# Optimization experiments

Hardware: AMD Instinct MI355X
Metric: run time of the kernel (lower is better)

## Reference

```python
import jax, jax.numpy as jnp
import numpy as np

N_NODES = 50000
N_EDGES = 800000
IN_DIM = 128
HID = 64
OUT = 64
HEADS = 4
NEG_SLOPE = 0.2  # DGL GATConv default leaky_relu negative slope


def gat_conv(x, src, dst, W, attn_l, attn_r, bias, n_heads, d_out, n_nodes):
    """DGL-style GATConv: x [N, F_in] -> [N, H, D]."""
    feat = (x @ W).reshape(n_nodes, n_heads, d_out)            # [N,H,D]
    el = jnp.sum(feat * attn_l, axis=-1)                        # [N,H]
    er = jnp.sum(feat * attn_r, axis=-1)                        # [N,H]
    e = jax.nn.leaky_relu(el[src] + er[dst], NEG_SLOPE)         # [E,H]
    # edge softmax over incoming edges of each dst node
    emax = jax.ops.segment_max(e, dst, num_segments=n_nodes)    # [N,H]
    emax = jnp.where(jnp.isfinite(emax), emax, 0.0)
    emax = jax.lax.stop_gradient(emax)
    a = jnp.exp(e - emax[dst])                                  # [E,H]
    denom = jax.ops.segment_sum(a, dst, num_segments=n_nodes)   # [N,H]
    alpha = a / jnp.maximum(denom[dst], 1e-9)                   # [E,H]
    msg = feat[src] * alpha[:, :, None]                         # [E,H,D]
    out = jax.ops.segment_sum(msg, dst, num_segments=n_nodes)   # [N,H,D]
    return out + bias.reshape(1, n_heads, d_out)


def setup_inputs() -> dict:
    key = jax.random.key(0)
    ks = jax.random.split(key, 12)
    features = jax.random.normal(ks[0], (N_NODES, IN_DIM), jnp.float32)
    src = jax.random.randint(ks[1], (N_EDGES,), 0, N_NODES)
    dst = jax.random.randint(ks[2], (N_EDGES,), 0, N_NODES)
    s1 = 1.0 / np.sqrt(IN_DIM)
    s2 = 1.0 / np.sqrt(HID * HEADS)
    return {
        "features": features,
        "src": src,
        "dst": dst,
        "W1": jax.random.normal(ks[3], (IN_DIM, HEADS * HID), jnp.float32) * s1,
        "al1": jax.random.normal(ks[4], (HEADS, HID), jnp.float32) * s1,
        "ar1": jax.random.normal(ks[5], (HEADS, HID), jnp.float32) * s1,
        "b1": jnp.zeros((HEADS * HID,), jnp.float32),
        "W2": jax.random.normal(ks[6], (HEADS * HID, HEADS * OUT), jnp.float32) * s2,
        "al2": jax.random.normal(ks[7], (HEADS, OUT), jnp.float32) * s2,
        "ar2": jax.random.normal(ks[8], (HEADS, OUT), jnp.float32) * s2,
        "b2": jnp.zeros((HEADS * OUT,), jnp.float32),
    }


def reference(features, src, dst, W1, al1, ar1, b1, W2, al2, ar2, b2):
    h = gat_conv(features, src, dst, W1, al1, ar1, b1, HEADS, HID, N_NODES)
    h = jax.nn.elu(h)                        # layer1 activation=F.elu
    h = h.reshape(N_NODES, HEADS * HID)      # .flatten(1)
    # dropout(0.2) is identity in eval mode
    h = gat_conv(h, src, dst, W2, al2, ar2, b2, HEADS, OUT, N_NODES)
    return h.mean(axis=1)                    # mean over heads -> [N, OUT]
```

## Files before the change

kernel.cpp:

```cpp
#include <hip/hip_runtime.h>
#include <hip/hip_bf16.h>
#include <math.h>

#define N_NODES 50000
#define N_EDGES 800000
#define IN_DIM 128
#define NEG_SLOPE 0.2f

typedef __attribute__((ext_vector_type(8))) short s16x8;
typedef __attribute__((ext_vector_type(4))) float f32x4;

__device__ inline unsigned short f2bf(float v) {
    unsigned u = __float_as_uint(v);
    unsigned r = (u + 0x7fffu + ((u >> 16) & 1u)) >> 16;
    return (unsigned short)r;
}
__device__ inline float bf2f(unsigned short b) {
    return __uint_as_float(((unsigned)b) << 16);
}
__device__ inline float lrelu(float v) {
    return v >= 0.f ? v : NEG_SLOPE * v;
}


__global__ void zero_int(int* __restrict__ p, int n) {
    int i = blockIdx.x * blockDim.x + threadIdx.x;
    if (i < n) p[i] = 0;
}

__global__ void hist_kernel(const int* __restrict__ dst, int* __restrict__ cnt) {
    int e = blockIdx.x * blockDim.x + threadIdx.x;
    if (e < N_EDGES) atomicAdd(&cnt[dst[e]], 1);
}

__global__ __launch_bounds__(1024) void scan_kernel(const int* __restrict__ cnt,
                                                    int* __restrict__ off, int n) {
    __shared__ int wsum[16];
    __shared__ int carry_s;
    int tid = threadIdx.x, wid = tid >> 6, lane = tid & 63;
    if (tid == 0) carry_s = 0;
    __syncthreads();
    for (int base = 0; base < n; base += 1024) {
        int i = base + tid;
        int v = (i < n) ? cnt[i] : 0;
        int x = v;
#pragma unroll
        for (int s = 1; s < 64; s <<= 1) {
            int t = __shfl_up(x, s, 64);
            if (lane >= s) x += t;
        }
        if (lane == 63) wsum[wid] = x;
        __syncthreads();
        if (wid == 0 && lane < 16) {
            int w = wsum[lane];
#pragma unroll
            for (int s = 1; s < 16; s <<= 1) {
                int t = __shfl_up(w, s, 64);
                if (lane >= s) w += t;
            }
            wsum[lane] = w;
        }
        __syncthreads();
        int woff = (wid > 0) ? wsum[wid - 1] : 0;
        int incl = carry_s + woff + x;
        if (i < n) off[i] = incl - v;
        __syncthreads();
        if (tid == 1023) carry_s = incl;
        __syncthreads();
    }
    if (threadIdx.x == 0) off[n] = carry_s;
}

__global__ void copy_int(const int* __restrict__ a, int* __restrict__ b, int n) {
    int i = blockIdx.x * blockDim.x + threadIdx.x;
    if (i < n) b[i] = a[i];
}

__global__ void scatter_kernel(const int* __restrict__ src, const int* __restrict__ dst,
                               int* __restrict__ cur, int* __restrict__ csr_src) {
    int e = blockIdx.x * blockDim.x + threadIdx.x;
    if (e < N_EDGES) {
        int d = dst[e];
        int pos = atomicAdd(&cur[d], 1);
        csr_src[pos] = src[e];
    }
}


__global__ void split_feat(const float* __restrict__ in, unsigned short* __restrict__ hi,
                           unsigned short* __restrict__ lo, int n4) {
    int i = blockIdx.x * blockDim.x + threadIdx.x;
    if (i < n4) {
        float4 v = *reinterpret_cast<const float4*>(&in[i * 4]);
        ushort4 h, l;
        h.x = f2bf(v.x); l.x = f2bf(v.x - bf2f(h.x));
        h.y = f2bf(v.y); l.y = f2bf(v.y - bf2f(h.y));
        h.z = f2bf(v.z); l.z = f2bf(v.z - bf2f(h.z));
        h.w = f2bf(v.w); l.w = f2bf(v.w - bf2f(h.w));
        *reinterpret_cast<ushort4*>(&hi[i * 4]) = h;
        *reinterpret_cast<ushort4*>(&lo[i * 4]) = l;
    }
}

template <int K>
__global__ void split_wt(const float* __restrict__ W, unsigned short* __restrict__ Bth,
                         unsigned short* __restrict__ Btl) {
    int k = blockIdx.x;
    int c = threadIdx.x;
    int h = c >> 6, w = c & 63;
    int row = h * 64 + (w & 3) * 16 + (w >> 2);
    float v = W[(size_t)k * 256 + c];
    unsigned short hh = f2bf(v);
    Bth[(size_t)row * K + k] = hh;
    Btl[(size_t)row * K + k] = f2bf(v - bf2f(hh));
}

template <int K>
__global__ void wlr_kernel(const float* __restrict__ W, const float* __restrict__ al,
                           const float* __restrict__ ar,
                           unsigned short* __restrict__ EhC, unsigned short* __restrict__ ElC) {
    int k = blockIdx.x * blockDim.x + threadIdx.x;
    if (k >= K) return;
#pragma unroll
    for (int h = 0; h < 4; h++) {
        float sl = 0.f, sr = 0.f;
        for (int c = 0; c < 64; c++) {
            float w = W[(size_t)k * 256 + h * 64 + c];
            sl += w * al[h * 64 + c];
            sr += w * ar[h * 64 + c];
        }
        unsigned short hh = f2bf(sl);
        EhC[(size_t)(h * 2 + 0) * K + k] = hh;
        ElC[(size_t)(h * 2 + 0) * K + k] = f2bf(sl - bf2f(hh));
        hh = f2bf(sr);
        EhC[(size_t)(h * 2 + 1) * K + k] = hh;
        ElC[(size_t)(h * 2 + 1) * K + k] = f2bf(sr - bf2f(hh));
    }
}


#define GLDS(gsrc, loff)                                                        \
    __builtin_amdgcn_global_load_lds(                                           \
        (const __attribute__((address_space(1))) unsigned int*)(gsrc),          \
        (__attribute__((address_space(3))) unsigned int*)(lds + (loff)),        \
        16, 0, 0)

template <int K>
__global__ __launch_bounds__(512) void mfma_gemm(const unsigned short* __restrict__ Ahi,
                                                 const unsigned short* __restrict__ Alo,
                                                 const unsigned short* __restrict__ Bth,
                                                 const unsigned short* __restrict__ Btl,
                                                 const unsigned short* __restrict__ EhC,
                                                 const unsigned short* __restrict__ ElC,
                                                 unsigned short* __restrict__ Chi,
                                                 float* __restrict__ el,
                                                 float* __restrict__ er,
                                                 int M) {
    __shared__ __align__(16) char lds[98304];
    int tid = threadIdx.x;
    int w = tid >> 6;
    int h = w & 3;
    int r2 = w >> 2;
    int lane = tid & 63;
    int rr = lane & 15;
    int g = lane >> 4;
    int row0 = blockIdx.x * 128;

    int arow = row0 + (tid & 127);
    if (arow >= M) arow = M - 1;
    int akc = (tid >> 7) & 3;
    const unsigned short* asrc_h = Ahi + (size_t)arow * K + akc * 8;
    const unsigned short* asrc_l = Alo + (size_t)arow * K + akc * 8;
    int btrow = tid & 255;
    int bkc = (tid >> 8) * 2;
    const unsigned short* bsrc_h = Bth + (size_t)btrow * K + bkc * 8;
    const unsigned short* bsrc_l = Btl + (size_t)btrow * K + bkc * 8;
    int bdst0 = 16384 + bkc * 4096 + btrow * 16;
    int bdst1 = 16384 + (bkc + 1) * 4096 + btrow * 16;

    f32x4 acc[4][4] = {};
    f32x4 acce[4] = {};

    GLDS(asrc_h, tid * 16);
    GLDS(asrc_l, 8192 + tid * 16);
    GLDS(bsrc_h, bdst0);
    GLDS(bsrc_h + 8, bdst1);
    GLDS(bsrc_l, 16384 + bdst0);
    GLDS(bsrc_l + 8, 16384 + bdst1);

    int cur = 0;
    for (int kb = 0; kb < K; kb += 32) {
        __syncthreads();
        if (kb + 32 < K) {
            int nb = (cur ^ 1) * 49152;
            GLDS(asrc_h + kb + 32, nb + tid * 16);
            GLDS(asrc_l + kb + 32, nb + 8192 + tid * 16);
            GLDS(bsrc_h + kb + 32, nb + bdst0);
            GLDS(bsrc_h + kb + 40, nb + bdst1);
            GLDS(bsrc_l + kb + 32, nb + 16384 + bdst0);
            GLDS(bsrc_l + kb + 40, nb + 16384 + bdst1);
        }
        s16x8 ehf = {};
        s16x8 elf = {};
        if (rr < 2) {
            ehf = *reinterpret_cast<const s16x8*>(EhC + (size_t)(h * 2 + rr) * K + kb + g * 8);
            elf = *reinterpret_cast<const s16x8*>(ElC + (size_t)(h * 2 + rr) * K + kb + g * 8);
        }
        const char* lb = lds + cur * 49152;
        s16x8 ah[4], al[4], bh[4], bl[4];
#pragma unroll
        for (int mi = 0; mi < 4; mi++) {
            int off = g * 2048 + (r2 * 64 + mi * 16 + rr) * 16;
            ah[mi] = *reinterpret_cast<const s16x8*>(lb + off);
            al[mi] = *reinterpret_cast<const s16x8*>(lb + 8192 + off);
        }
#pragma unroll
        for (int ni = 0; ni < 4; ni++) {
            int off = g * 4096 + (h * 64 + ni * 16 + rr) * 16;
            bh[ni] = *reinterpret_cast<const s16x8*>(lb + 16384 + off);
            bl[ni] = *reinterpret_cast<const s16x8*>(lb + 32768 + off);
        }
#pragma unroll
        for (int mi = 0; mi < 4; mi++) {
#pragma unroll
            for (int ni = 0; ni < 4; ni++) {
                acc[mi][ni] = __builtin_amdgcn_mfma_f32_16x16x32_bf16(ah[mi], bh[ni], acc[mi][ni], 0, 0, 0);
                acc[mi][ni] = __builtin_amdgcn_mfma_f32_16x16x32_bf16(ah[mi], bl[ni], acc[mi][ni], 0, 0, 0);
                acc[mi][ni] = __builtin_amdgcn_mfma_f32_16x16x32_bf16(al[mi], bh[ni], acc[mi][ni], 0, 0, 0);
            }
            acce[mi] = __builtin_amdgcn_mfma_f32_16x16x32_bf16(ah[mi], ehf, acce[mi], 0, 0, 0);
            acce[mi] = __builtin_amdgcn_mfma_f32_16x16x32_bf16(ah[mi], elf, acce[mi], 0, 0, 0);
            acce[mi] = __builtin_amdgcn_mfma_f32_16x16x32_bf16(al[mi], ehf, acce[mi], 0, 0, 0);
        }
        cur ^= 1;
    }

#pragma unroll
    for (int mi = 0; mi < 4; mi++) {
#pragma unroll
        for (int reg = 0; reg < 4; reg++) {
            int row = row0 + r2 * 64 + mi * 16 + g * 4 + reg;
            if (row < M) {
                ushort4 u;
                u.x = f2bf(acc[mi][0][reg]);
                u.y = f2bf(acc[mi][1][reg]);
                u.z = f2bf(acc[mi][2][reg]);
                u.w = f2bf(acc[mi][3][reg]);
                *reinterpret_cast<ushort4*>(&Chi[(size_t)row * 256 + h * 64 + rr * 4]) = u;
                if (rr == 0) el[row * 4 + h] = acce[mi][reg];
                if (rr == 1) er[row * 4 + h] = acce[mi][reg];
            }
        }
    }
}


template <int LAYER>
__global__ __launch_bounds__(256) void agg_kernel(const unsigned short* __restrict__ feat16,
                                                  const float* __restrict__ el,
                                                  const float* __restrict__ er,
                                                  const int* __restrict__ row_off,
                                                  const int* __restrict__ csr_src,
                                                  const float* __restrict__ bias,
                                                  unsigned short* __restrict__ out_hi,
                                                  unsigned short* __restrict__ out_lo,
                                                  float* __restrict__ outf) {
    int n = blockIdx.x * 4 + (threadIdx.x >> 6);
    int lane = threadIdx.x & 63;
    int h = lane >> 4;
    int js = row_off[n], je = row_off[n + 1];
    float er_nh = er[n * 4 + h];
    float m = -INFINITY, ssum = 0.f;
    float4 acc = make_float4(0.f, 0.f, 0.f, 0.f);
    int j = js;
    for (; j + 7 < je; j += 8) {
        int ss[8]; ushort4 uu[8]; float vv[8];
#pragma unroll
        for (int q = 0; q < 8; q++) ss[q] = csr_src[j + q];
#pragma unroll
        for (int q = 0; q < 8; q++)
            uu[q] = *reinterpret_cast<const ushort4*>(&feat16[(size_t)ss[q] * 256 + lane * 4]);
#pragma unroll
        for (int q = 0; q < 8; q++) vv[q] = lrelu(el[ss[q] * 4 + h] + er_nh);
        float mx = fmaxf(fmaxf(fmaxf(vv[0], vv[1]), fmaxf(vv[2], vv[3])),
                         fmaxf(fmaxf(vv[4], vv[5]), fmaxf(vv[6], vv[7])));
        float mn = fmaxf(m, mx);
        float sc = __expf(m - mn);
        float p[8];
#pragma unroll
        for (int q = 0; q < 8; q++) p[q] = __expf(vv[q] - mn);
        float psum = ((p[0] + p[1]) + (p[2] + p[3])) + ((p[4] + p[5]) + (p[6] + p[7]));
        ssum = ssum * sc + psum;
        float ax = 0.f, ay = 0.f, az = 0.f, aw = 0.f;
#pragma unroll
        for (int q = 0; q < 8; q++) {
            ax += p[q] * bf2f(uu[q].x);
            ay += p[q] * bf2f(uu[q].y);
            az += p[q] * bf2f(uu[q].z);
            aw += p[q] * bf2f(uu[q].w);
        }
        acc.x = acc.x * sc + ax;
        acc.y = acc.y * sc + ay;
        acc.z = acc.z * sc + az;
        acc.w = acc.w * sc + aw;
        m = mn;
    }
    for (; j + 3 < je; j += 4) {
        int s0 = csr_src[j], s1 = csr_src[j + 1], s2 = csr_src[j + 2], s3 = csr_src[j + 3];
        ushort4 u0 = *reinterpret_cast<const ushort4*>(&feat16[(size_t)s0 * 256 + lane * 4]);
        ushort4 u1 = *reinterpret_cast<const ushort4*>(&feat16[(size_t)s1 * 256 + lane * 4]);
        ushort4 u2 = *reinterpret_cast<const ushort4*>(&feat16[(size_t)s2 * 256 + lane * 4]);
        ushort4 u3 = *reinterpret_cast<const ushort4*>(&feat16[(size_t)s3 * 256 + lane * 4]);
        float v0 = lrelu(el[s0 * 4 + h] + er_nh);
        float v1 = lrelu(el[s1 * 4 + h] + er_nh);
        float v2 = lrelu(el[s2 * 4 + h] + er_nh);
        float v3 = lrelu(el[s3 * 4 + h] + er_nh);
        float mx = fmaxf(fmaxf(v0, v1), fmaxf(v2, v3));
        float mn = fmaxf(m, mx);
        float sc = __expf(m - mn);
        float p0 = __expf(v0 - mn);
        float p1 = __expf(v1 - mn);
        float p2 = __expf(v2 - mn);
        float p3 = __expf(v3 - mn);
        ssum = ssum * sc + ((p0 + p1) + (p2 + p3));
        acc.x = acc.x * sc + (p0 * bf2f(u0.x) + p1 * bf2f(u1.x)) + (p2 * bf2f(u2.x) + p3 * bf2f(u3.x));
        acc.y = acc.y * sc + (p0 * bf2f(u0.y) + p1 * bf2f(u1.y)) + (p2 * bf2f(u2.y) + p3 * bf2f(u3.y));
        acc.z = acc.z * sc + (p0 * bf2f(u0.z) + p1 * bf2f(u1.z)) + (p2 * bf2f(u2.z) + p3 * bf2f(u3.z));
        acc.w = acc.w * sc + (p0 * bf2f(u0.w) + p1 * bf2f(u1.w)) + (p2 * bf2f(u2.w) + p3 * bf2f(u3.w));
        m = mn;
    }
    for (; j < je; j++) {
        int s = csr_src[j];
        ushort4 u = *reinterpret_cast<const ushort4*>(&feat16[(size_t)s * 256 + lane * 4]);
        float val = lrelu(el[s * 4 + h] + er_nh);
        float mn = fmaxf(m, val);
        float sc = __expf(m - mn);
        float p = __expf(val - mn);
        ssum = ssum * sc + p;
        acc.x = acc.x * sc + p * bf2f(u.x);
        acc.y = acc.y * sc + p * bf2f(u.y);
        acc.z = acc.z * sc + p * bf2f(u.z);
        acc.w = acc.w * sc + p * bf2f(u.w);
        m = mn;
    }
    float inv = 1.f / fmaxf(ssum, 1e-9f);
    float4 res;
    res.x = acc.x * inv + bias[lane * 4 + 0];
    res.y = acc.y * inv + bias[lane * 4 + 1];
    res.z = acc.z * inv + bias[lane * 4 + 2];
    res.w = acc.w * inv + bias[lane * 4 + 3];
    if (LAYER == 1) {
        res.x = res.x > 0.f ? res.x : __expf(res.x) - 1.f;
        res.y = res.y > 0.f ? res.y : __expf(res.y) - 1.f;
        res.z = res.z > 0.f ? res.z : __expf(res.z) - 1.f;
        res.w = res.w > 0.f ? res.w : __expf(res.w) - 1.f;
        ushort4 hz, lz;
        hz.x = f2bf(res.x); lz.x = f2bf(res.x - bf2f(hz.x));
        hz.y = f2bf(res.y); lz.y = f2bf(res.y - bf2f(hz.y));
        hz.z = f2bf(res.z); lz.z = f2bf(res.z - bf2f(hz.z));
        hz.w = f2bf(res.w); lz.w = f2bf(res.w - bf2f(hz.w));
        *reinterpret_cast<ushort4*>(&out_hi[(size_t)n * 256 + lane * 4]) = hz;
        *reinterpret_cast<ushort4*>(&out_lo[(size_t)n * 256 + lane * 4]) = lz;
    } else {
#pragma unroll
        for (int mask = 16; mask <= 32; mask <<= 1) {
            res.x += __shfl_xor(res.x, mask, 64);
            res.y += __shfl_xor(res.y, mask, 64);
            res.z += __shfl_xor(res.z, mask, 64);
            res.w += __shfl_xor(res.w, mask, 64);
        }
        if (lane < 16) {
            float4 o = make_float4(res.x * 0.25f, res.y * 0.25f, res.z * 0.25f, res.w * 0.25f);
            *reinterpret_cast<float4*>(&outf[(size_t)n * 64 + lane * 4]) = o;
        }
    }
}


extern "C" void kernel_launch(void* const* d_in, const int* in_sizes, int n_in,
                              void* d_out, int out_size, void* d_ws, size_t ws_size,
                              hipStream_t stream) {
    const float* features = (const float*)d_in[0];
    const int*   src      = (const int*)d_in[1];
    const int*   dst      = (const int*)d_in[2];
    const float* W1       = (const float*)d_in[3];
    const float* al1      = (const float*)d_in[4];
    const float* ar1      = (const float*)d_in[5];
    const float* b1       = (const float*)d_in[6];
    const float* W2       = (const float*)d_in[7];
    const float* al2      = (const float*)d_in[8];
    const float* ar2      = (const float*)d_in[9];
    const float* b2       = (const float*)d_in[10];
    float* out = (float*)d_out;

    char* ws = (char*)d_ws;
    unsigned short* feat16  = (unsigned short*)(ws);
    unsigned short* h1_hi   = (unsigned short*)(ws + 25600000);
    unsigned short* h1_lo   = (unsigned short*)(ws + 51200000);
    unsigned short* fA_hi   = (unsigned short*)(ws + 76800000);
    unsigned short* fA_lo   = (unsigned short*)(ws + 89600000);
    unsigned short* Bt1_hi  = (unsigned short*)(ws + 102400000);
    unsigned short* Bt1_lo  = (unsigned short*)(ws + 102465536);
    unsigned short* Bt2_hi  = (unsigned short*)(ws + 102531072);
    unsigned short* Bt2_lo  = (unsigned short*)(ws + 102662144);
    unsigned short* E1C_hi  = (unsigned short*)(ws + 102793216);
    unsigned short* E1C_lo  = (unsigned short*)(ws + 102795264);
    unsigned short* E2C_hi  = (unsigned short*)(ws + 102797312);
    unsigned short* E2C_lo  = (unsigned short*)(ws + 102801408);
    float*          el      = (float*)(ws + 102805504);
    float*          er      = (float*)(ws + 103605504);
    int*            row_off = (int*)  (ws + 104405504);
    int*            cur     = (int*)  (ws + 104605568);
    int*            csr     = (int*)  (ws + 104805568);

    zero_int<<<(N_NODES + 255) / 256, 256, 0, stream>>>(cur, N_NODES);
    hist_kernel<<<(N_EDGES + 255) / 256, 256, 0, stream>>>(dst, cur);
    scan_kernel<<<1, 1024, 0, stream>>>(cur, row_off, N_NODES);
    copy_int<<<(N_NODES + 255) / 256, 256, 0, stream>>>(row_off, cur, N_NODES);
    scatter_kernel<<<(N_EDGES + 255) / 256, 256, 0, stream>>>(src, dst, cur, csr);

    split_feat<<<(N_NODES * IN_DIM / 4 + 255) / 256, 256, 0, stream>>>(
        features, fA_hi, fA_lo, N_NODES * IN_DIM / 4);
    split_wt<IN_DIM><<<IN_DIM, 256, 0, stream>>>(W1, Bt1_hi, Bt1_lo);
    split_wt<256><<<256, 256, 0, stream>>>(W2, Bt2_hi, Bt2_lo);
    wlr_kernel<IN_DIM><<<1, IN_DIM, 0, stream>>>(W1, al1, ar1, E1C_hi, E1C_lo);
    wlr_kernel<256><<<1, 256, 0, stream>>>(W2, al2, ar2, E2C_hi, E2C_lo);

    int gemm_blocks = (N_NODES + 127) / 128;

    mfma_gemm<IN_DIM><<<gemm_blocks, 512, 0, stream>>>(
        fA_hi, fA_lo, Bt1_hi, Bt1_lo, E1C_hi, E1C_lo, feat16, el, er, N_NODES);
    agg_kernel<1><<<12500, 256, 0, stream>>>(feat16, el, er, row_off, csr, b1, h1_hi, h1_lo, nullptr);

    mfma_gemm<256><<<gemm_blocks, 512, 0, stream>>>(
        h1_hi, h1_lo, Bt2_hi, Bt2_lo, E2C_hi, E2C_lo, feat16, el, er, N_NODES);
    agg_kernel<2><<<12500, 256, 0, stream>>>(feat16, el, er, row_off, csr, b2, nullptr, nullptr, out);
}
```

Before: 391.0 us.

## Parallelize CSR scan, fuse fp32 split into GEMM, split edge aggregation across waves

```diff
diff --git a/kernel.cpp b/kernel.cpp
--- a/kernel.cpp
+++ b/kernel.cpp
@@ -33,47 +33,72 @@
     if (e < N_EDGES) atomicAdd(&cnt[dst[e]], 1);
 }
 
-__global__ __launch_bounds__(1024) void scan_kernel(const int* __restrict__ cnt,
-                                                    int* __restrict__ off, int n) {
-    __shared__ int wsum[16];
-    __shared__ int carry_s;
-    int tid = threadIdx.x, wid = tid >> 6, lane = tid & 63;
-    if (tid == 0) carry_s = 0;
+__global__ __launch_bounds__(256) void scan_part(const int* __restrict__ cnt,
+                                                 int* __restrict__ off,
+                                                 int* __restrict__ part, int n) {
+    __shared__ int wsum[4];
+    int t = threadIdx.x, wid = t >> 6, lane = t & 63;
+    int i = blockIdx.x * 256 + t;
+    int v = (i < n) ? cnt[i] : 0;
+    int x = v;
+#pragma unroll
+    for (int s = 1; s < 64; s <<= 1) {
+        int u = __shfl_up(x, s, 64);
+        if (lane >= s) x += u;
+    }
+    if (lane == 63) wsum[wid] = x;
     __syncthreads();
-    for (int base = 0; base < n; base += 1024) {
-        int i = base + tid;
-        int v = (i < n) ? cnt[i] : 0;
-        int x = v;
-#pragma unroll
-        for (int s = 1; s < 64; s <<= 1) {
-            int t = __shfl_up(x, s, 64);
-            if (lane >= s) x += t;
-        }
-        if (lane == 63) wsum[wid] = x;
-        __syncthreads();
-        if (wid == 0 && lane < 16) {
-            int w = wsum[lane];
-#pragma unroll
-            for (int s = 1; s < 16; s <<= 1) {
-                int t = __shfl_up(w, s, 64);
-                if (lane >= s) w += t;
-            }
-            wsum[lane] = w;
-        }
-        __syncthreads();
-        int woff = (wid > 0) ? wsum[wid - 1] : 0;
-        int incl = carry_s + woff + x;
-        if (i < n) off[i] = incl - v;
-        __syncthreads();
-        if (tid == 1023) carry_s = incl;
-        __syncthreads();
-    }
-    if (threadIdx.x == 0) off[n] = carry_s;
-}
-
-__global__ void copy_int(const int* __restrict__ a, int* __restrict__ b, int n) {
+    if (t < 4) {
+        int w = wsum[t];
+#pragma unroll
+        for (int s = 1; s < 4; s <<= 1) {
+            int u = __shfl_up(w, s, 64);
+            if (t >= s) w += u;
+        }
+        wsum[t] = w;
+    }
+    __syncthreads();
+    int woff = (wid > 0) ? wsum[wid - 1] : 0;
+    int incl = woff + x;
+    if (i < n) off[i] = incl - v;
+    if (t == 255) part[blockIdx.x] = incl;
+}
+
+__global__ __launch_bounds__(256) void scan_carry(int* __restrict__ part, int nb) {
+    __shared__ int wsum[4];
+    int t = threadIdx.x, wid = t >> 6, lane = t & 63;
+    int v = (t < nb) ? part[t] : 0;
+    int x = v;
+#pragma unroll
+    for (int s = 1; s < 64; s <<= 1) {
+        int u = __shfl_up(x, s, 64);
+        if (lane >= s) x += u;
+    }
+    if (lane == 63) wsum[wid] = x;
+    __syncthreads();
+    if (t < 4) {
+        int w = wsum[t];
+#pragma unroll
+        for (int s = 1; s < 4; s <<= 1) {
+            int u = __shfl_up(w, s, 64);
+            if (t >= s) w += u;
+        }
+        wsum[t] = w;
+    }
+    __syncthreads();
+    int woff = (wid > 0) ? wsum[wid - 1] : 0;
+    if (t < nb) part[t] = woff + x - v;
+}
+
+__global__ void scan_add(int* __restrict__ off, const int* __restrict__ part,
+                         int* __restrict__ cur, int n) {
     int i = blockIdx.x * blockDim.x + threadIdx.x;
-    if (i < n) b[i] = a[i];
+    if (i < n) {
+        int val = off[i] + part[i >> 8];
+        off[i] = val;
+        cur[i] = val;
+    }
+    if (i == 0) off[n] = N_EDGES;
 }
 
 __global__ void scatter_kernel(const int* __restrict__ src, const int* __restrict__ dst,
@@ -86,21 +111,6 @@
     }
 }
 
-
-__global__ void split_feat(const float* __restrict__ in, unsigned short* __restrict__ hi,
-                           unsigned short* __restrict__ lo, int n4) {
-    int i = blockIdx.x * blockDim.x + threadIdx.x;
-    if (i < n4) {
-        float4 v = *reinterpret_cast<const float4*>(&in[i * 4]);
-        ushort4 h, l;
-        h.x = f2bf(v.x); l.x = f2bf(v.x - bf2f(h.x));
-        h.y = f2bf(v.y); l.y = f2bf(v.y - bf2f(h.y));
-        h.z = f2bf(v.z); l.z = f2bf(v.z - bf2f(h.z));
-        h.w = f2bf(v.w); l.w = f2bf(v.w - bf2f(h.w));
-        *reinterpret_cast<ushort4*>(&hi[i * 4]) = h;
-        *reinterpret_cast<ushort4*>(&lo[i * 4]) = l;
-    }
-}
 
 template <int K>
 __global__ void split_wt(const float* __restrict__ W, unsigned short* __restrict__ Bth,
@@ -145,8 +155,8 @@
         (__attribute__((address_space(3))) unsigned int*)(lds + (loff)),        \
         16, 0, 0)
 
-template <int K>
-__global__ __launch_bounds__(512) void mfma_gemm(const unsigned short* __restrict__ Ahi,
+template <int K, bool AF32>
+__global__ __launch_bounds__(512) void mfma_gemm(const void* __restrict__ A_,
                                                  const unsigned short* __restrict__ Alo,
                                                  const unsigned short* __restrict__ Bth,
                                                  const unsigned short* __restrict__ Btl,
@@ -168,8 +178,13 @@
 
     int arow = row0 + (tid & 127);
     if (arow >= M) arow = M - 1;
+    const float* Af = (const float*)A_;
+    const unsigned short* Ah = (const unsigned short*)A_;
+    int fg = (tid >> 7) & 3;
+    const float* afsrc0 = Af + (size_t)arow * K + fg * 4;
+    const float* afsrc1 = Af + (size_t)arow * K + (fg + 4) * 4;
     int akc = (tid >> 7) & 3;
-    const unsigned short* asrc_h = Ahi + (size_t)arow * K + akc * 8;
+    const unsigned short* asrc_h = Ah + (size_t)arow * K + akc * 8;
     const unsigned short* asrc_l = Alo + (size_t)arow * K + akc * 8;
     int btrow = tid & 255;
     int bkc = (tid >> 8) * 2;
@@ -181,8 +196,13 @@
     f32x4 acc[4][4] = {};
     f32x4 acce[4] = {};
 
-    GLDS(asrc_h, tid * 16);
-    GLDS(asrc_l, 8192 + tid * 16);
+    if (AF32) {
+        GLDS(afsrc0, tid * 16);
+        GLDS(afsrc1, 8192 + tid * 16);
+    } else {
+        GLDS(asrc_h, tid * 16);
+        GLDS(asrc_l, 8192 + tid * 16);
+    }
     GLDS(bsrc_h, bdst0);
     GLDS(bsrc_h + 8, bdst1);
     GLDS(bsrc_l, 16384 + bdst0);
@@ -193,8 +213,13 @@
         __syncthreads();
         if (kb + 32 < K) {
             int nb = (cur ^ 1) * 49152;
-            GLDS(asrc_h + kb + 32, nb + tid * 16);
-            GLDS(asrc_l + kb + 32, nb + 8192 + tid * 16);
+            if (AF32) {
+                GLDS(afsrc0 + kb + 32, nb + tid * 16);
+                GLDS(afsrc1 + kb + 32, nb + 8192 + tid * 16);
+            } else {
+                GLDS(asrc_h + kb + 32, nb + tid * 16);
+                GLDS(asrc_l + kb + 32, nb + 8192 + tid * 16);
+            }
             GLDS(bsrc_h + kb + 32, nb + bdst0);
             GLDS(bsrc_h + kb + 40, nb + bdst1);
             GLDS(bsrc_l + kb + 32, nb + 16384 + bdst0);
@@ -210,9 +235,22 @@
         s16x8 ah[4], al[4], bh[4], bl[4];
 #pragma unroll
         for (int mi = 0; mi < 4; mi++) {
-            int off = g * 2048 + (r2 * 64 + mi * 16 + rr) * 16;
-            ah[mi] = *reinterpret_cast<const s16x8*>(lb + off);
-            al[mi] = *reinterpret_cast<const s16x8*>(lb + 8192 + off);
+            int row = r2 * 64 + mi * 16 + rr;
+            if (AF32) {
+                float4 f0 = *reinterpret_cast<const float4*>(lb + g * 4096 + row * 16);
+                float4 f1 = *reinterpret_cast<const float4*>(lb + g * 4096 + 2048 + row * 16);
+                float vv[8] = {f0.x, f0.y, f0.z, f0.w, f1.x, f1.y, f1.z, f1.w};
+#pragma unroll
+                for (int i = 0; i < 8; i++) {
+                    unsigned short hh = f2bf(vv[i]);
+                    ah[mi][i] = (short)hh;
+                    al[mi][i] = (short)f2bf(vv[i] - bf2f(hh));
+                }
+            } else {
+                int off = g * 2048 + row * 16;
+                ah[mi] = *reinterpret_cast<const s16x8*>(lb + off);
+                al[mi] = *reinterpret_cast<const s16x8*>(lb + 8192 + off);
+            }
         }
 #pragma unroll
         for (int ni = 0; ni < 4; ni++) {
@@ -255,8 +293,12 @@
 }
 
 
+__device__ inline float lse_scale(float x, float mt) {
+    return (x <= -3.0e38f) ? 0.f : __expf(x - mt);
+}
+
 template <int LAYER>
-__global__ __launch_bounds__(256) void agg_kernel(const unsigned short* __restrict__ feat16,
+__global__ __launch_bounds__(512) void agg_kernel(const unsigned short* __restrict__ feat16,
                                                   const float* __restrict__ el,
                                                   const float* __restrict__ er,
                                                   const int* __restrict__ row_off,
@@ -265,10 +307,18 @@
                                                   unsigned short* __restrict__ out_hi,
                                                   unsigned short* __restrict__ out_lo,
                                                   float* __restrict__ outf) {
-    int n = blockIdx.x * 4 + (threadIdx.x >> 6);
+    __shared__ float lm[8][64];
+    __shared__ float ls[8][64];
+    __shared__ float lacc[8][64][4];
+    int w = threadIdx.x >> 6;
     int lane = threadIdx.x & 63;
+    int n = blockIdx.x * 4 + (w & 3);
+    int half = w >> 2;
     int h = lane >> 4;
-    int js = row_off[n], je = row_off[n + 1];
+    int js0 = row_off[n], je0 = row_off[n + 1];
+    int mid = js0 + ((je0 - js0 + 1) >> 1);
+    int js = half ? mid : js0;
+    int je = half ? je0 : mid;
     float er_nh = er[n * 4 + h];
     float m = -INFINITY, ssum = 0.f;
     float4 acc = make_float4(0.f, 0.f, 0.f, 0.f);
@@ -343,12 +393,31 @@
         acc.w = acc.w * sc + p * bf2f(u.w);
         m = mn;
     }
-    float inv = 1.f / fmaxf(ssum, 1e-9f);
+
+    lm[w][lane] = m;
+    ls[w][lane] = ssum;
+    lacc[w][lane][0] = acc.x;
+    lacc[w][lane][1] = acc.y;
+    lacc[w][lane][2] = acc.z;
+    lacc[w][lane][3] = acc.w;
+    __syncthreads();
+    if (w >= 4) return;
+    float mB = lm[w + 4][lane];
+    float sB = ls[w + 4][lane];
+    float mt = fmaxf(m, mB);
+    float fA = lse_scale(m, mt);
+    float fB = lse_scale(mB, mt);
+    float ssum_t = ssum * fA + sB * fB;
     float4 res;
-    res.x = acc.x * inv + bias[lane * 4 + 0];
-    res.y = acc.y * inv + bias[lane * 4 + 1];
-    res.z = acc.z * inv + bias[lane * 4 + 2];
-    res.w = acc.w * inv + bias[lane * 4 + 3];
+    res.x = acc.x * fA + lacc[w + 4][lane][0] * fB;
+    res.y = acc.y * fA + lacc[w + 4][lane][1] * fB;
+    res.z = acc.z * fA + lacc[w + 4][lane][2] * fB;
+    res.w = acc.w * fA + lacc[w + 4][lane][3] * fB;
+    float inv = 1.f / fmaxf(ssum_t, 1e-9f);
+    res.x = res.x * inv + bias[lane * 4 + 0];
+    res.y = res.y * inv + bias[lane * 4 + 1];
+    res.z = res.z * inv + bias[lane * 4 + 2];
+    res.w = res.w * inv + bias[lane * 4 + 3];
     if (LAYER == 1) {
         res.x = res.x > 0.f ? res.x : __expf(res.x) - 1.f;
         res.y = res.y > 0.f ? res.y : __expf(res.y) - 1.f;
@@ -397,30 +466,29 @@
     unsigned short* feat16  = (unsigned short*)(ws);
     unsigned short* h1_hi   = (unsigned short*)(ws + 25600000);
     unsigned short* h1_lo   = (unsigned short*)(ws + 51200000);
-    unsigned short* fA_hi   = (unsigned short*)(ws + 76800000);
-    unsigned short* fA_lo   = (unsigned short*)(ws + 89600000);
-    unsigned short* Bt1_hi  = (unsigned short*)(ws + 102400000);
-    unsigned short* Bt1_lo  = (unsigned short*)(ws + 102465536);
-    unsigned short* Bt2_hi  = (unsigned short*)(ws + 102531072);
-    unsigned short* Bt2_lo  = (unsigned short*)(ws + 102662144);
-    unsigned short* E1C_hi  = (unsigned short*)(ws + 102793216);
-    unsigned short* E1C_lo  = (unsigned short*)(ws + 102795264);
-    unsigned short* E2C_hi  = (unsigned short*)(ws + 102797312);
-    unsigned short* E2C_lo  = (unsigned short*)(ws + 102801408);
-    float*          el      = (float*)(ws + 102805504);
-    float*          er      = (float*)(ws + 103605504);
-    int*            row_off = (int*)  (ws + 104405504);
-    int*            cur     = (int*)  (ws + 104605568);
-    int*            csr     = (int*)  (ws + 104805568);
+    unsigned short* Bt1_hi  = (unsigned short*)(ws + 76800000);
+    unsigned short* Bt1_lo  = (unsigned short*)(ws + 76865536);
+    unsigned short* Bt2_hi  = (unsigned short*)(ws + 76931072);
+    unsigned short* Bt2_lo  = (unsigned short*)(ws + 77062144);
+    unsigned short* E1C_hi  = (unsigned short*)(ws + 77193216);
+    unsigned short* E1C_lo  = (unsigned short*)(ws + 77195264);
+    unsigned short* E2C_hi  = (unsigned short*)(ws + 77197312);
+    unsigned short* E2C_lo  = (unsigned short*)(ws + 77201408);
+    float*          el      = (float*)(ws + 77205504);
+    float*          er      = (float*)(ws + 78005504);
+    int*            row_off = (int*)  (ws + 78805504);
+    int*            cur     = (int*)  (ws + 79005568);
+    int*            part    = (int*)  (ws + 79205568);
+    int*            csr     = (int*)  (ws + 79206592);
 
     zero_int<<<(N_NODES + 255) / 256, 256, 0, stream>>>(cur, N_NODES);
     hist_kernel<<<(N_EDGES + 255) / 256, 256, 0, stream>>>(dst, cur);
-    scan_kernel<<<1, 1024, 0, stream>>>(cur, row_off, N_NODES);
-    copy_int<<<(N_NODES + 255) / 256, 256, 0, stream>>>(row_off, cur, N_NODES);
+    int nb = (N_NODES + 255) / 256;
+    scan_part<<<nb, 256, 0, stream>>>(cur, row_off, part, N_NODES);
+    scan_carry<<<1, 256, 0, stream>>>(part, nb);
+    scan_add<<<(N_NODES + 255) / 256, 256, 0, stream>>>(row_off, part, cur, N_NODES);
     scatter_kernel<<<(N_EDGES + 255) / 256, 256, 0, stream>>>(src, dst, cur, csr);
 
-    split_feat<<<(N_NODES * IN_DIM / 4 + 255) / 256, 256, 0, stream>>>(
-        features, fA_hi, fA_lo, N_NODES * IN_DIM / 4);
     split_wt<IN_DIM><<<IN_DIM, 256, 0, stream>>>(W1, Bt1_hi, Bt1_lo);
     split_wt<256><<<256, 256, 0, stream>>>(W2, Bt2_hi, Bt2_lo);
     wlr_kernel<IN_DIM><<<1, IN_DIM, 0, stream>>>(W1, al1, ar1, E1C_hi, E1C_lo);
@@ -428,11 +496,11 @@
 
     int gemm_blocks = (N_NODES + 127) / 128;
 
-    mfma_gemm<IN_DIM><<<gemm_blocks, 512, 0, stream>>>(
-        fA_hi, fA_lo, Bt1_hi, Bt1_lo, E1C_hi, E1C_lo, feat16, el, er, N_NODES);
-    agg_kernel<1><<<12500, 256, 0, stream>>>(feat16, el, er, row_off, csr, b1, h1_hi, h1_lo, nullptr);
-
-    mfma_gemm<256><<<gemm_blocks, 512, 0, stream>>>(
+    mfma_gemm<IN_DIM, true><<<gemm_blocks, 512, 0, stream>>>(
+        features, nullptr, Bt1_hi, Bt1_lo, E1C_hi, E1C_lo, feat16, el, er, N_NODES);
+    agg_kernel<1><<<12500, 512, 0, stream>>>(feat16, el, er, row_off, csr, b1, h1_hi, h1_lo, nullptr);
+
+    mfma_gemm<256, false><<<gemm_blocks, 512, 0, stream>>>(
         h1_hi, h1_lo, Bt2_hi, Bt2_lo, E2C_hi, E2C_lo, feat16, el, er, N_NODES);
-    agg_kernel<2><<<12500, 256, 0, stream>>>(feat16, el, er, row_off, csr, b2, nullptr, nullptr, out);
-}
+    agg_kernel<2><<<12500, 512, 0, stream>>>(feat16, el, er, row_off, csr, b2, nullptr, nullptr, out);
+}
```

Result: no change. 384.9 us (-1.6%).
